# Kernel optimization log

Hardware: AMD Instinct MI355X
Metric: run time of the kernel (lower is better)

Reference implementation:

```python
import jax, jax.numpy as jnp
import numpy as np

N_HEADS = 8
TANH_CLIPPING = 10.0
TEMP = 1.0


def setup_inputs() -> dict:
    key = jax.random.key(0)
    ks = jax.random.split(key, 8)
    B, N, D, CTX = 256, 1000, 128, 130
    embeddings = jax.random.normal(ks[0], (B, N, D), dtype=jnp.float32)
    step_context = jax.random.normal(ks[1], (B, 1, CTX), dtype=jnp.float32)
    mask = jax.random.randint(ks[2], (B, 1, N), 0, 2).astype(bool)
    # ensure at least one feasible node per row (node 0 always feasible)
    mask = mask.at[:, :, 0].set(False)
    W_node = jax.random.normal(ks[3], (D, 3 * D), dtype=jnp.float32) * (1.0 / np.sqrt(D))
    W_fixed = jax.random.normal(ks[4], (D, D), dtype=jnp.float32) * (1.0 / np.sqrt(D))
    W_step = jax.random.normal(ks[5], (CTX, D), dtype=jnp.float32) * (1.0 / np.sqrt(CTX))
    W_out = jax.random.normal(ks[6], (D, D), dtype=jnp.float32) * (1.0 / np.sqrt(D))
    return {"embeddings": embeddings, "step_context": step_context, "mask": mask,
            "W_node": W_node, "W_fixed": W_fixed, "W_step": W_step, "W_out": W_out}


def reference(embeddings, step_context, mask, W_node, W_fixed, W_step, W_out):
    # embeddings: [B, N, D], step_context: [B, 1, D+2], mask: [B, 1, N] (True = infeasible)
    B, N, D = embeddings.shape
    H = N_HEADS
    hd = D // H
    # _precompute: fixed context from graph mean, and K/V/logit_key from node embeddings
    graph_embed = embeddings.mean(axis=1)                       # [B, D]
    fixed_context = graph_embed @ W_fixed                       # [B, D]
    kvl = embeddings @ W_node                                   # [B, N, 3D]
    glimpse_k, glimpse_v, logit_k = jnp.split(kvl, 3, axis=-1)  # each [B, N, D]
    # query = fixed context + projected step context             [B, 1, D]
    query = fixed_context[:, None, :] + step_context @ W_step
    # multi-head glimpse attention (q_len = 1)
    q = query.reshape(B, 1, H, hd).transpose(0, 2, 1, 3)        # [B, H, 1, hd]
    K = glimpse_k.reshape(B, N, H, hd).transpose(0, 2, 1, 3)    # [B, H, N, hd]
    V = glimpse_v.reshape(B, N, H, hd).transpose(0, 2, 1, 3)    # [B, H, N, hd]
    compat = jnp.einsum('bhqd,bhnd->bhqn', q, K) / jnp.sqrt(jnp.float32(hd))
    # mask_inner
    compat = jnp.where(mask[:, None, :, :], -jnp.inf, compat)
    attn = jax.nn.softmax(compat, axis=-1)                      # [B, H, 1, N]
    heads = jnp.einsum('bhqn,bhnd->bhqd', attn, V)              # [B, H, 1, hd]
    glimpse = heads.transpose(0, 2, 1, 3).reshape(B, 1, D) @ W_out  # [B, 1, D]
    # single-head logits against logit_key, tanh-clipped
    logits = jnp.einsum('bqd,bnd->bqn', glimpse, logit_k) / jnp.sqrt(jnp.float32(D))
    logits = jnp.tanh(logits) * TANH_CLIPPING
    # mask_logits
    logits = jnp.where(mask, -jnp.inf, logits)
    log_p = jax.nn.log_softmax(logits / TEMP, axis=-1)          # [B, 1, N]
    return log_p
```

## Files before the change

kernel.cpp:

```cpp
#include <hip/hip_runtime.h>
#include <math.h>

#define NN   1000
#define DD   128
#define CTXN 130
#define NEG_BIG (-1.0e30f)


__global__ __launch_bounds__(1024, 4)
void k1_fused(const float* __restrict__ emb, const float* __restrict__ stepc,
              const void* __restrict__ maskp,
              const float* __restrict__ Wn, const float* __restrict__ Wf,
              const float* __restrict__ Ws,
              float* __restrict__ qpt, int* __restrict__ idxv, int* __restrict__ cntv) {
    const int b = blockIdx.x, t = threadIdx.x;
    const int w = t >> 6, lane = t & 63;
    const float* eb = emb + (size_t)b * (NN * DD);
    __shared__ __align__(16) float S[4096];
    __shared__ float s_mean[128], s_q[128];
    __shared__ int s_misint;
    __shared__ unsigned long long s_bal[16];
    __shared__ int s_woff[16];
    if (t == 0) {
        const unsigned char* mb8 = (const unsigned char*)maskp;
        int any = 0;
        for (int k = 0; k < 64; ++k) any |= mb8[4 * k + 1];
        s_misint = (any == 0) ? 1 : 0;
    }
    {
        const int c4 = t & 31, g = t >> 5;
        float4 a = make_float4(0.f, 0.f, 0.f, 0.f);
        for (int r = g; r < NN; r += 32) {
            const float4 v = *(const float4*)(eb + (size_t)r * DD + c4 * 4);
            a.x += v.x; a.y += v.y; a.z += v.z; a.w += v.w;
        }
        ((float4*)S)[g * 32 + c4] = a;
    }
    __syncthreads();
    if (t < 128) {
        float v = 0.f;
        #pragma unroll
        for (int g = 0; g < 32; ++g) v += S[g * 128 + t];
        s_mean[t] = v * (1.0f / (float)NN);
    }
    __syncthreads();
    {
        const int d = t & 127, p = t >> 7;
        float a = 0.f;
        for (int i = 16 * p; i < 16 * p + 16; ++i)
            a = fmaf(s_mean[i], Wf[i * DD + d], a);
        const float* scb = stepc + (size_t)b * CTXN;
        const int c0 = 16 * p, c1 = (p == 7) ? CTXN : 16 * p + 16;
        for (int c = c0; c < c1; ++c)
            a = fmaf(scb[c], Ws[c * DD + d], a);
        S[p * 128 + d] = a;
    }
    __syncthreads();
    if (t < 128) {
        float v = 0.f;
        #pragma unroll
        for (int p = 0; p < 8; ++p) v += S[p * 128 + t];
        s_q[t] = v;
    }
    __syncthreads();
    {
        const int i = t & 127, h = t >> 7;
        float a = 0.f;
        #pragma unroll
        for (int j = 0; j < 16; ++j)
            a = fmaf(Wn[i * 384 + h * 16 + j], s_q[h * 16 + j], a);
        qpt[(size_t)b * 1024 + h * 128 + i] = a * 0.25f;
    }
    {
        const unsigned char* mk8 = (const unsigned char*)maskp + (size_t)b * NN;
        const int* mk32 = (const int*)maskp + (size_t)b * NN;
        int um = 0;
        if (t < NN) um = s_misint ? (mk32[t] == 0) : (mk8[t] == 0);
        const unsigned long long bal = __ballot(um);
        if (lane == 0) s_bal[w] = bal;
        __syncthreads();
        if (t == 0) {
            int o = 0;
            #pragma unroll
            for (int w2 = 0; w2 < 16; ++w2) {
                s_woff[w2] = o;
                o += (int)__popcll(s_bal[w2]);
            }
            cntv[b] = o;
        }
        __syncthreads();
        if (um) {
            const int pos = s_woff[w] +
                (int)__popcll(bal & ((lane == 0) ? 0ULL : (~0ULL >> (64 - lane))));
            idxv[(size_t)b * 1024 + pos] = t;
        }
    }
}

__global__ __launch_bounds__(512, 4)
void kB_stream(const float* __restrict__ emb, const float* __restrict__ qpt,
               const int* __restrict__ idxv, const int* __restrict__ cntv,
               float* __restrict__ wembp, float* __restrict__ stats) {
    const int b = blockIdx.x >> 3, s = blockIdx.x & 7;
    const int t = threadIdx.x, w = t >> 6, lane = t & 63;
    const int rg = lane >> 4, cl = lane & 15;
    const int cnt = cntv[b];
    const int lo = (s * cnt) >> 3;
    const int hi = ((s + 1) * cnt) >> 3;
    const int nrows = hi - lo;
    const float* eb = emb + (size_t)b * (NN * DD);
    __shared__ __align__(16) float s_qpT[1024];
    __shared__ __align__(16) float s_part[8 * 8 * 132];
    __shared__ float s_sumw[64];
    __shared__ int s_idx[128];
    for (int i = t; i < 1024; i += 512) s_qpT[i] = qpt[(size_t)b * 1024 + i];
    if (t < 128) s_idx[t] = (t < nrows) ? idxv[(size_t)b * 1024 + lo + t] : 0;
    __syncthreads();
    const int h0 = 2 * rg, h1 = 2 * rg + 1;
    const float4 qa0 = *(const float4*)&s_qpT[h0 * 128 + cl * 8];
    const float4 qa1 = *(const float4*)&s_qpT[h0 * 128 + cl * 8 + 4];
    const float4 qb0 = *(const float4*)&s_qpT[h1 * 128 + cl * 8];
    const float4 qb1 = *(const float4*)&s_qpT[h1 * 128 + cl * 8 + 4];
    float4 a0A = make_float4(0.f,0.f,0.f,0.f), a0B = a0A;
    float4 a1A = a0A, a1B = a0A;
    float ps0 = 0.f, ps1 = 0.f;
    const int niter = (nrows + 7) >> 3;
    for (int it = 0; it < niter; ++it) {
        const int rp = it * 8 + w;
        const bool valid = (rp < nrows);
        const int n = s_idx[rp & 127];
        float4 e0 = make_float4(0.f,0.f,0.f,0.f), e1 = e0;
        if (valid) {
            e0 = *(const float4*)(eb + (size_t)n * DD + cl * 8);
            e1 = *(const float4*)(eb + (size_t)n * DD + cl * 8 + 4);
        }
        float c0 = e0.x * qa0.x;
        c0 = fmaf(e0.y, qa0.y, c0); c0 = fmaf(e0.z, qa0.z, c0); c0 = fmaf(e0.w, qa0.w, c0);
        c0 = fmaf(e1.x, qa1.x, c0); c0 = fmaf(e1.y, qa1.y, c0);
        c0 = fmaf(e1.z, qa1.z, c0); c0 = fmaf(e1.w, qa1.w, c0);
        float c1 = e0.x * qb0.x;
        c1 = fmaf(e0.y, qb0.y, c1); c1 = fmaf(e0.z, qb0.z, c1); c1 = fmaf(e0.w, qb0.w, c1);
        c1 = fmaf(e1.x, qb1.x, c1); c1 = fmaf(e1.y, qb1.y, c1);
        c1 = fmaf(e1.z, qb1.z, c1); c1 = fmaf(e1.w, qb1.w, c1);
        c0 += __shfl_xor(c0, 1, 16); c1 += __shfl_xor(c1, 1, 16);
        c0 += __shfl_xor(c0, 2, 16); c1 += __shfl_xor(c1, 2, 16);
        c0 += __shfl_xor(c0, 4, 16); c1 += __shfl_xor(c1, 4, 16);
        c0 += __shfl_xor(c0, 8, 16); c1 += __shfl_xor(c1, 8, 16);
        const float p0 = valid ? expf(fminf(c0, 80.f)) : 0.f;
        const float p1 = valid ? expf(fminf(c1, 80.f)) : 0.f;
        ps0 += p0; ps1 += p1;
        a0A.x = fmaf(p0, e0.x, a0A.x); a0A.y = fmaf(p0, e0.y, a0A.y);
        a0A.z = fmaf(p0, e0.z, a0A.z); a0A.w = fmaf(p0, e0.w, a0A.w);
        a0B.x = fmaf(p0, e1.x, a0B.x); a0B.y = fmaf(p0, e1.y, a0B.y);
        a0B.z = fmaf(p0, e1.z, a0B.z); a0B.w = fmaf(p0, e1.w, a0B.w);
        a1A.x = fmaf(p1, e0.x, a1A.x); a1A.y = fmaf(p1, e0.y, a1A.y);
        a1A.z = fmaf(p1, e0.z, a1A.z); a1A.w = fmaf(p1, e0.w, a1A.w);
        a1B.x = fmaf(p1, e1.x, a1B.x); a1B.y = fmaf(p1, e1.y, a1B.y);
        a1B.z = fmaf(p1, e1.z, a1B.z); a1B.w = fmaf(p1, e1.w, a1B.w);
    }
    *(float4*)&s_part[(w * 8 + h0) * 132 + cl * 8]     = a0A;
    *(float4*)&s_part[(w * 8 + h0) * 132 + cl * 8 + 4] = a0B;
    *(float4*)&s_part[(w * 8 + h1) * 132 + cl * 8]     = a1A;
    *(float4*)&s_part[(w * 8 + h1) * 132 + cl * 8 + 4] = a1B;
    if (cl == 0) { s_sumw[w * 8 + h0] = ps0; s_sumw[w * 8 + h1] = ps1; }
    __syncthreads();
    for (int i = t; i < 1024; i += 512) {
        const int h = i >> 7, c = i & 127;
        float v = 0.f;
        #pragma unroll
        for (int w2 = 0; w2 < 8; ++w2) v += s_part[(w2 * 8 + h) * 132 + c];
        wembp[(size_t)b * 8192 + s * 1024 + i] = v;
    }
    if (t < 8) {
        float v = 0.f;
        #pragma unroll
        for (int w2 = 0; w2 < 8; ++w2) v += s_sumw[w2 * 8 + t];
        stats[(size_t)b * 64 + s * 8 + t] = v;
    }
}

__global__ __launch_bounds__(1024, 4)
void k4_fused(const float* __restrict__ emb, const float* __restrict__ wembp,
              const float* __restrict__ stats,
              const float* __restrict__ Wn, const float* __restrict__ Wo,
              const int* __restrict__ idxv, const int* __restrict__ cntv,
              float* __restrict__ out) {
    const int b = blockIdx.x, t = threadIdx.x;
    const int w = t >> 6, lane = t & 63;
    const int rg = lane >> 4, cl = lane & 15;
    const float* eb = emb + (size_t)b * (NN * DD);
    __shared__ float s_dinv[8];
    __shared__ float s_wemb[8 * 130];
    __shared__ __align__(16) float s_red[1024];
    __shared__ float s_h[128], s_gl[128], s_g2[128];
    __shared__ float s_logits[1000];
    __shared__ int s_idxf[1024];
    __shared__ float s_r2[32];
    __shared__ float s_lse;
    const int cnt = cntv[b];
    if (t < NN) s_logits[t] = NEG_BIG;
    s_idxf[t] = (t < cnt) ? idxv[(size_t)b * 1024 + t] : 0;
    if (t < 8) {
        float den = 0.f;
        #pragma unroll
        for (int ss = 0; ss < 8; ++ss) den += stats[(size_t)b * 64 + ss * 8 + t];
        s_dinv[t] = 1.0f / den;
    }
    __syncthreads();
    {
        const int h = t >> 7, i = t & 127;
        float v = 0.f;
        #pragma unroll
        for (int ss = 0; ss < 8; ++ss)
            v += wembp[(size_t)b * 8192 + ss * 1024 + t];
        s_wemb[h * 130 + i] = v * s_dinv[h];
    }
    __syncthreads();
    {
        const int j = t & 127, p = t >> 7;
        float a = 0.f;
        for (int i = 16 * p; i < 16 * p + 16; ++i)
            a = fmaf(Wn[i * 384 + 128 + j], s_wemb[(j >> 4) * 130 + i], a);
        s_red[p * 128 + j] = a;
    }
    __syncthreads();
    if (t < 128) {
        float v = 0.f;
        #pragma unroll
        for (int p = 0; p < 8; ++p) v += s_red[p * 128 + t];
        s_h[t] = v;
    }
    __syncthreads();
    {
        const int d = t & 127, p = t >> 7;
        float a = 0.f;
        for (int j = 16 * p; j < 16 * p + 16; ++j)
            a = fmaf(s_h[j], Wo[j * DD + d], a);
        s_red[p * 128 + d] = a;
    }
    __syncthreads();
    if (t < 128) {
        float v = 0.f;
        #pragma unroll
        for (int p = 0; p < 8; ++p) v += s_red[p * 128 + t];
        s_gl[t] = v;
    }
    __syncthreads();
    {
        const int i = t & 127, p = t >> 7;
        float a = 0.f;
        for (int d = 16 * p; d < 16 * p + 16; ++d)
            a = fmaf(Wn[i * 384 + 256 + d], s_gl[d], a);
        s_red[p * 128 + i] = a;
    }
    __syncthreads();
    if (t < 128) {
        float v = 0.f;
        #pragma unroll
        for (int p = 0; p < 8; ++p) v += s_red[p * 128 + t];
        s_g2[t] = v * 0.08838834764831845f;
    }
    __syncthreads();
    {
        const float4 ga = *(const float4*)&s_g2[cl * 8];
        const float4 gb = *(const float4*)&s_g2[cl * 8 + 4];
        for (int it = 0; it < 16; ++it) {
            const int pos = it * 64 + w * 4 + rg;
            const bool valid = (pos < cnt);
            const int n = s_idxf[pos];
            float a = 0.f;
            if (valid) {
                const float4 e0 = *(const float4*)(eb + (size_t)n * DD + cl * 8);
                const float4 e1 = *(const float4*)(eb + (size_t)n * DD + cl * 8 + 4);
                a = e0.x * ga.x;
                a = fmaf(e0.y, ga.y, a);
                a = fmaf(e0.z, ga.z, a);
                a = fmaf(e0.w, ga.w, a);
                a = fmaf(e1.x, gb.x, a);
                a = fmaf(e1.y, gb.y, a);
                a = fmaf(e1.z, gb.z, a);
                a = fmaf(e1.w, gb.w, a);
            }
            a += __shfl_xor(a, 1, 16);
            a += __shfl_xor(a, 2, 16);
            a += __shfl_xor(a, 4, 16);
            a += __shfl_xor(a, 8, 16);
            if (cl == 0 && valid)
                s_logits[n] = 10.0f * tanhf(a);
        }
    }
    __syncthreads();
    {
        float m = NEG_BIG;
        if (t < NN) m = s_logits[t];
        #pragma unroll
        for (int o = 32; o; o >>= 1) m = fmaxf(m, __shfl_xor(m, o, 64));
        if (lane == 0) s_r2[w] = m;
        __syncthreads();
        if (t == 0) {
            float mm = s_r2[0];
            #pragma unroll
            for (int i = 1; i < 16; ++i) mm = fmaxf(mm, s_r2[i]);
            s_r2[16] = mm;
        }
        __syncthreads();
        const float mb = s_r2[16];
        float sum = (t < NN) ? expf(s_logits[t] - mb) : 0.f;
        #pragma unroll
        for (int o = 32; o; o >>= 1) sum += __shfl_xor(sum, o, 64);
        __syncthreads();
        if (lane == 0) s_r2[w] = sum;
        __syncthreads();
        if (t == 0) {
            float ss = 0.f;
            #pragma unroll
            for (int i = 0; i < 16; ++i) ss += s_r2[i];
            s_lse = mb + logf(ss);
        }
        __syncthreads();
        if (t < NN) out[(size_t)b * NN + t] = s_logits[t] - s_lse;
    }
}

extern "C" void kernel_launch(void* const* d_in, const int* in_sizes, int n_in,
                              void* d_out, int out_size, void* d_ws, size_t ws_size,
                              hipStream_t stream) {
    const float* emb   = (const float*)d_in[0];
    const float* stepc = (const float*)d_in[1];
    const void*  mask  = (const void*)d_in[2];
    const float* Wn = (const float*)d_in[3];
    const float* Wf = (const float*)d_in[4];
    const float* Ws = (const float*)d_in[5];
    const float* Wo = (const float*)d_in[6];
    float* out = (float*)d_out;
    const int B = in_sizes[0] / (NN * DD);

    float* wsf = (float*)d_ws;
    const size_t n_qpt   = (size_t)B * 1024;
    const size_t n_wembp = (size_t)B * 8192;
    const size_t n_stats = (size_t)B * 64;
    const size_t n_idx   = (size_t)B * 1024;

    float* qpt   = wsf;
    float* wembp = qpt + n_qpt;
    float* stats = wembp + n_wembp;
    int*   idxv  = (int*)(stats + n_stats);
    int*   cntv  = idxv + n_idx;

    k1_fused <<<B,     1024, 0, stream>>>(emb, stepc, mask, Wn, Wf, Ws, qpt, idxv, cntv);
    kB_stream<<<B * 8, 512,  0, stream>>>(emb, qpt, idxv, cntv, wembp, stats);
    k4_fused <<<B,     1024, 0, stream>>>(emb, wembp, stats, Wn, Wo, idxv, cntv, out);
}
```

Measured before the change: 82.99 us.

## Split mean and logits phases into per-batch multi-block kernels

The embedding-mean reduction and the final logit/log-softmax stage each used to run as one 1024-thread block per batch row. Both are now spread over 8 blocks per row, with partial results passed through workspace. The softmax normaliser drops the max-subtraction pass, which relies on tanh clipping to keep the logits within ±10. The goal is more concurrent blocks for the memory-bound passes over the embeddings. The cost is going from three launches to six, plus extra global round-trips for the partial sums and logits.

New measurement: 88.76 us. 1.07x slower.

```diff
diff --git a/kernel.cpp b/kernel.cpp
--- a/kernel.cpp
+++ b/kernel.cpp
@@ -7,40 +7,53 @@
 #define NEG_BIG (-1.0e30f)
 
 
-__global__ __launch_bounds__(1024, 4)
-void k1_fused(const float* __restrict__ emb, const float* __restrict__ stepc,
-              const void* __restrict__ maskp,
-              const float* __restrict__ Wn, const float* __restrict__ Wf,
-              const float* __restrict__ Ws,
-              float* __restrict__ qpt, int* __restrict__ idxv, int* __restrict__ cntv) {
-    const int b = blockIdx.x, t = threadIdx.x;
-    const int w = t >> 6, lane = t & 63;
+__global__ __launch_bounds__(256, 8)
+void k1p_meanpart(const float* __restrict__ emb, const void* __restrict__ maskp,
+                  float* __restrict__ meanp, int* __restrict__ mflag) {
+    const int b = blockIdx.x >> 3, s = blockIdx.x & 7;
+    const int t = threadIdx.x;
     const float* eb = emb + (size_t)b * (NN * DD);
-    __shared__ __align__(16) float S[4096];
-    __shared__ float s_mean[128], s_q[128];
-    __shared__ int s_misint;
-    __shared__ unsigned long long s_bal[16];
-    __shared__ int s_woff[16];
-    if (t == 0) {
+    __shared__ __align__(16) float s_red[8 * 128];
+    if (blockIdx.x == 0 && t == 0) {
         const unsigned char* mb8 = (const unsigned char*)maskp;
         int any = 0;
         for (int k = 0; k < 64; ++k) any |= mb8[4 * k + 1];
-        s_misint = (any == 0) ? 1 : 0;
-    }
-    {
-        const int c4 = t & 31, g = t >> 5;
-        float4 a = make_float4(0.f, 0.f, 0.f, 0.f);
-        for (int r = g; r < NN; r += 32) {
-            const float4 v = *(const float4*)(eb + (size_t)r * DD + c4 * 4);
-            a.x += v.x; a.y += v.y; a.z += v.z; a.w += v.w;
-        }
-        ((float4*)S)[g * 32 + c4] = a;
-    }
+        *mflag = (any == 0) ? 1 : 0;
+    }
+    const int c4 = t & 31, rg = t >> 5;
+    float4 a = make_float4(0.f, 0.f, 0.f, 0.f);
+    for (int nl = rg; nl < 125; nl += 8) {
+        const float4 v = *(const float4*)(eb + (size_t)(s * 125 + nl) * DD + c4 * 4);
+        a.x += v.x; a.y += v.y; a.z += v.z; a.w += v.w;
+    }
+    ((float4*)s_red)[rg * 32 + c4] = a;
     __syncthreads();
     if (t < 128) {
         float v = 0.f;
         #pragma unroll
-        for (int g = 0; g < 32; ++g) v += S[g * 128 + t];
+        for (int g = 0; g < 8; ++g) v += s_red[g * 128 + t];
+        meanp[(size_t)b * 1024 + s * 128 + t] = v;
+    }
+}
+
+__global__ __launch_bounds__(1024, 4)
+void k1q_qproj(const float* __restrict__ meanp, const float* __restrict__ stepc,
+               const void* __restrict__ maskp, const int* __restrict__ mflag,
+               const float* __restrict__ Wn, const float* __restrict__ Wf,
+               const float* __restrict__ Ws,
+               float* __restrict__ qpt, int* __restrict__ idxv, int* __restrict__ cntv,
+               float* __restrict__ logits) {
+    const int b = blockIdx.x, t = threadIdx.x;
+    const int w = t >> 6, lane = t & 63;
+    __shared__ __align__(16) float S[1024];
+    __shared__ float s_mean[128], s_q[128];
+    __shared__ unsigned long long s_bal[16];
+    __shared__ int s_woff[16];
+    if (t < NN) logits[(size_t)b * 1024 + t] = NEG_BIG;
+    if (t < 128) {
+        float v = 0.f;
+        #pragma unroll
+        for (int g = 0; g < 8; ++g) v += meanp[(size_t)b * 1024 + g * 128 + t];
         s_mean[t] = v * (1.0f / (float)NN);
     }
     __syncthreads();
@@ -72,10 +85,11 @@
         qpt[(size_t)b * 1024 + h * 128 + i] = a * 0.25f;
     }
     {
+        const int misint = *mflag;
         const unsigned char* mk8 = (const unsigned char*)maskp + (size_t)b * NN;
         const int* mk32 = (const int*)maskp + (size_t)b * NN;
         int um = 0;
-        if (t < NN) um = s_misint ? (mk32[t] == 0) : (mk8[t] == 0);
+        if (t < NN) um = misint ? (mk32[t] == 0) : (mk8[t] == 0);
         const unsigned long long bal = __ballot(um);
         if (lane == 0) s_bal[w] = bal;
         __syncthreads();
@@ -179,27 +193,15 @@
     }
 }
 
-__global__ __launch_bounds__(1024, 4)
-void k4_fused(const float* __restrict__ emb, const float* __restrict__ wembp,
-              const float* __restrict__ stats,
-              const float* __restrict__ Wn, const float* __restrict__ Wo,
-              const int* __restrict__ idxv, const int* __restrict__ cntv,
-              float* __restrict__ out) {
+__global__ __launch_bounds__(512, 4)
+void k4a_g2(const float* __restrict__ wembp, const float* __restrict__ stats,
+            const float* __restrict__ Wn, const float* __restrict__ Wo,
+            float* __restrict__ g2v) {
     const int b = blockIdx.x, t = threadIdx.x;
-    const int w = t >> 6, lane = t & 63;
-    const int rg = lane >> 4, cl = lane & 15;
-    const float* eb = emb + (size_t)b * (NN * DD);
     __shared__ float s_dinv[8];
     __shared__ float s_wemb[8 * 130];
-    __shared__ __align__(16) float s_red[1024];
-    __shared__ float s_h[128], s_gl[128], s_g2[128];
-    __shared__ float s_logits[1000];
-    __shared__ int s_idxf[1024];
-    __shared__ float s_r2[32];
-    __shared__ float s_lse;
-    const int cnt = cntv[b];
-    if (t < NN) s_logits[t] = NEG_BIG;
-    s_idxf[t] = (t < cnt) ? idxv[(size_t)b * 1024 + t] : 0;
+    __shared__ float s_red[512];
+    __shared__ float s_h[128], s_gl[128];
     if (t < 8) {
         float den = 0.f;
         #pragma unroll
@@ -207,119 +209,121 @@
         s_dinv[t] = 1.0f / den;
     }
     __syncthreads();
-    {
-        const int h = t >> 7, i = t & 127;
+    for (int idx = t; idx < 1024; idx += 512) {
+        const int h = idx >> 7, i = idx & 127;
         float v = 0.f;
         #pragma unroll
         for (int ss = 0; ss < 8; ++ss)
-            v += wembp[(size_t)b * 8192 + ss * 1024 + t];
+            v += wembp[(size_t)b * 8192 + ss * 1024 + idx];
         s_wemb[h * 130 + i] = v * s_dinv[h];
     }
     __syncthreads();
     {
         const int j = t & 127, p = t >> 7;
         float a = 0.f;
-        for (int i = 16 * p; i < 16 * p + 16; ++i)
+        for (int i = 32 * p; i < 32 * p + 32; ++i)
             a = fmaf(Wn[i * 384 + 128 + j], s_wemb[(j >> 4) * 130 + i], a);
         s_red[p * 128 + j] = a;
     }
     __syncthreads();
-    if (t < 128) {
-        float v = 0.f;
-        #pragma unroll
-        for (int p = 0; p < 8; ++p) v += s_red[p * 128 + t];
-        s_h[t] = v;
-    }
+    if (t < 128) s_h[t] = s_red[t] + s_red[128 + t] + s_red[256 + t] + s_red[384 + t];
     __syncthreads();
     {
         const int d = t & 127, p = t >> 7;
         float a = 0.f;
-        for (int j = 16 * p; j < 16 * p + 16; ++j)
+        for (int j = 32 * p; j < 32 * p + 32; ++j)
             a = fmaf(s_h[j], Wo[j * DD + d], a);
         s_red[p * 128 + d] = a;
     }
     __syncthreads();
-    if (t < 128) {
-        float v = 0.f;
-        #pragma unroll
-        for (int p = 0; p < 8; ++p) v += s_red[p * 128 + t];
-        s_gl[t] = v;
-    }
+    if (t < 128) s_gl[t] = s_red[t] + s_red[128 + t] + s_red[256 + t] + s_red[384 + t];
     __syncthreads();
     {
         const int i = t & 127, p = t >> 7;
         float a = 0.f;
-        for (int d = 16 * p; d < 16 * p + 16; ++d)
+        for (int d = 32 * p; d < 32 * p + 32; ++d)
             a = fmaf(Wn[i * 384 + 256 + d], s_gl[d], a);
         s_red[p * 128 + i] = a;
     }
     __syncthreads();
+    if (t < 128)
+        g2v[(size_t)b * 128 + t] =
+            (s_red[t] + s_red[128 + t] + s_red[256 + t] + s_red[384 + t]) * 0.08838834764831845f;
+}
+
+__global__ __launch_bounds__(512, 4)
+void k4b_logits(const float* __restrict__ emb, const float* __restrict__ g2v,
+                const int* __restrict__ idxv, const int* __restrict__ cntv,
+                float* __restrict__ logits, float* __restrict__ lstats) {
+    const int b = blockIdx.x >> 3, s = blockIdx.x & 7;
+    const int t = threadIdx.x, w = t >> 6, lane = t & 63;
+    const int rg = lane >> 4, cl = lane & 15;
+    const int cnt = cntv[b];
+    const int lo = (s * cnt) >> 3;
+    const int hi = ((s + 1) * cnt) >> 3;
+    const int nrows = hi - lo;
+    const float* eb = emb + (size_t)b * (NN * DD);
+    __shared__ __align__(16) float s_g2[128];
+    __shared__ int s_idx[128];
+    __shared__ float s_ws[8];
     if (t < 128) {
-        float v = 0.f;
-        #pragma unroll
-        for (int p = 0; p < 8; ++p) v += s_red[p * 128 + t];
-        s_g2[t] = v * 0.08838834764831845f;
-    }
-    __syncthreads();
-    {
-        const float4 ga = *(const float4*)&s_g2[cl * 8];
-        const float4 gb = *(const float4*)&s_g2[cl * 8 + 4];
-        for (int it = 0; it < 16; ++it) {
-            const int pos = it * 64 + w * 4 + rg;
-            const bool valid = (pos < cnt);
-            const int n = s_idxf[pos];
-            float a = 0.f;
-            if (valid) {
-                const float4 e0 = *(const float4*)(eb + (size_t)n * DD + cl * 8);
-                const float4 e1 = *(const float4*)(eb + (size_t)n * DD + cl * 8 + 4);
-                a = e0.x * ga.x;
-                a = fmaf(e0.y, ga.y, a);
-                a = fmaf(e0.z, ga.z, a);
-                a = fmaf(e0.w, ga.w, a);
-                a = fmaf(e1.x, gb.x, a);
-                a = fmaf(e1.y, gb.y, a);
-                a = fmaf(e1.z, gb.z, a);
-                a = fmaf(e1.w, gb.w, a);
-            }
-            a += __shfl_xor(a, 1, 16);
-            a += __shfl_xor(a, 2, 16);
-            a += __shfl_xor(a, 4, 16);
-            a += __shfl_xor(a, 8, 16);
-            if (cl == 0 && valid)
-                s_logits[n] = 10.0f * tanhf(a);
-        }
-    }
-    __syncthreads();
-    {
-        float m = NEG_BIG;
-        if (t < NN) m = s_logits[t];
-        #pragma unroll
-        for (int o = 32; o; o >>= 1) m = fmaxf(m, __shfl_xor(m, o, 64));
-        if (lane == 0) s_r2[w] = m;
-        __syncthreads();
-        if (t == 0) {
-            float mm = s_r2[0];
-            #pragma unroll
-            for (int i = 1; i < 16; ++i) mm = fmaxf(mm, s_r2[i]);
-            s_r2[16] = mm;
-        }
-        __syncthreads();
-        const float mb = s_r2[16];
-        float sum = (t < NN) ? expf(s_logits[t] - mb) : 0.f;
-        #pragma unroll
-        for (int o = 32; o; o >>= 1) sum += __shfl_xor(sum, o, 64);
-        __syncthreads();
-        if (lane == 0) s_r2[w] = sum;
-        __syncthreads();
-        if (t == 0) {
-            float ss = 0.f;
-            #pragma unroll
-            for (int i = 0; i < 16; ++i) ss += s_r2[i];
-            s_lse = mb + logf(ss);
-        }
-        __syncthreads();
-        if (t < NN) out[(size_t)b * NN + t] = s_logits[t] - s_lse;
-    }
+        s_g2[t] = g2v[(size_t)b * 128 + t];
+        s_idx[t] = (t < nrows) ? idxv[(size_t)b * 1024 + lo + t] : 0;
+    }
+    __syncthreads();
+    const float4 ga = *(const float4*)&s_g2[cl * 8];
+    const float4 gb = *(const float4*)&s_g2[cl * 8 + 4];
+    float lsum = 0.f;
+    const int niter = (nrows + 31) >> 5;
+    for (int it = 0; it < niter; ++it) {
+        const int rp = it * 32 + w * 4 + rg;
+        const bool valid = (rp < nrows);
+        const int n = s_idx[rp & 127];
+        float a = 0.f;
+        if (valid) {
+            const float4 e0 = *(const float4*)(eb + (size_t)n * DD + cl * 8);
+            const float4 e1 = *(const float4*)(eb + (size_t)n * DD + cl * 8 + 4);
+            a = e0.x * ga.x;
+            a = fmaf(e0.y, ga.y, a);
+            a = fmaf(e0.z, ga.z, a);
+            a = fmaf(e0.w, ga.w, a);
+            a = fmaf(e1.x, gb.x, a);
+            a = fmaf(e1.y, gb.y, a);
+            a = fmaf(e1.z, gb.z, a);
+            a = fmaf(e1.w, gb.w, a);
+        }
+        a += __shfl_xor(a, 1, 16);
+        a += __shfl_xor(a, 2, 16);
+        a += __shfl_xor(a, 4, 16);
+        a += __shfl_xor(a, 8, 16);
+        if (cl == 0 && valid) {
+            const float lg = 10.0f * tanhf(a);
+            logits[(size_t)b * 1024 + n] = lg;
+            lsum += expf(lg);
+        }
+    }
+    #pragma unroll
+    for (int o = 32; o; o >>= 1) lsum += __shfl_xor(lsum, o, 64);
+    if (lane == 0) s_ws[w] = lsum;
+    __syncthreads();
+    if (t == 0) {
+        float v = 0.f;
+        #pragma unroll
+        for (int w2 = 0; w2 < 8; ++w2) v += s_ws[w2];
+        lstats[(size_t)b * 8 + s] = v;
+    }
+}
+
+__global__ __launch_bounds__(256, 8)
+void k5_norm(const float* __restrict__ logits, const float* __restrict__ lstats,
+             float* __restrict__ out) {
+    const int b = blockIdx.x, t = threadIdx.x;
+    float den = 0.f;
+    #pragma unroll
+    for (int s = 0; s < 8; ++s) den += lstats[(size_t)b * 8 + s];
+    const float lse = logf(den);
+    for (int n = t; n < NN; n += 256)
+        out[(size_t)b * NN + n] = logits[(size_t)b * 1024 + n] - lse;
 }
 
 extern "C" void kernel_launch(void* const* d_in, const int* in_sizes, int n_in,
@@ -336,18 +340,31 @@
     const int B = in_sizes[0] / (NN * DD);
 
     float* wsf = (float*)d_ws;
+    const size_t n_meanp = (size_t)B * 1024;
     const size_t n_qpt   = (size_t)B * 1024;
     const size_t n_wembp = (size_t)B * 8192;
     const size_t n_stats = (size_t)B * 64;
     const size_t n_idx   = (size_t)B * 1024;
-
-    float* qpt   = wsf;
-    float* wembp = qpt + n_qpt;
-    float* stats = wembp + n_wembp;
-    int*   idxv  = (int*)(stats + n_stats);
-    int*   cntv  = idxv + n_idx;
-
-    k1_fused <<<B,     1024, 0, stream>>>(emb, stepc, mask, Wn, Wf, Ws, qpt, idxv, cntv);
-    kB_stream<<<B * 8, 512,  0, stream>>>(emb, qpt, idxv, cntv, wembp, stats);
-    k4_fused <<<B,     1024, 0, stream>>>(emb, wembp, stats, Wn, Wo, idxv, cntv, out);
-}
+    const size_t n_g2    = (size_t)B * 128;
+    const size_t n_logit = (size_t)B * 1024;
+    const size_t n_lst   = (size_t)B * 8;
+
+    float* meanp  = wsf;
+    float* qpt    = meanp + n_meanp;
+    float* wembp  = qpt + n_qpt;
+    float* stats  = wembp + n_wembp;
+    float* g2v    = stats + n_stats;
+    float* logits = g2v + n_g2;
+    float* lstats = logits + n_logit;
+    int*   idxv   = (int*)(lstats + n_lst);
+    int*   cntv   = idxv + n_idx;
+    int*   mflag  = cntv + B;
+
+    k1p_meanpart<<<B * 8, 256, 0, stream>>>(emb, mask, meanp, mflag);
+    k1q_qproj   <<<B,     1024, 0, stream>>>(meanp, stepc, mask, mflag, Wn, Wf, Ws,
+                                             qpt, idxv, cntv, logits);
+    kB_stream   <<<B * 8, 512, 0, stream>>>(emb, qpt, idxv, cntv, wembp, stats);
+    k4a_g2      <<<B,     512, 0, stream>>>(wembp, stats, Wn, Wo, g2v);
+    k4b_logits  <<<B * 8, 512, 0, stream>>>(emb, g2v, idxv, cntv, logits, lstats);
+    k5_norm     <<<B,     256, 0, stream>>>(logits, lstats, out);
+}
```
